# Performance work log

Hardware: AMD Instinct MI355X
Metric: run time of the kernel (lower is better)

## Reference

```python
import jax, jax.numpy as jnp
import numpy as np

NEG = -65504.0
D = 640


def _linear(x, W, b):
    return x @ W + b


def _qkv_attention(q, k, v, mask4):
    # q:[B,Lq,D] k,v:[B,Lk,D] mask4:[B,1,1,Lk] (True = masked)
    scores = jnp.einsum('bqd,bkd->bqk', q, k) / jnp.sqrt(jnp.asarray(q.shape[-1], q.dtype))
    scores = jnp.where(mask4[:, 0, :, :], NEG, scores)  # mask.squeeze(1) -> [B,1,Lk]
    p = jax.nn.softmax(scores, axis=-1)
    return jnp.einsum('bqk,bkd->bqd', p, v)


def _attflat(x, mask4, W1, b1, W2, b2, Wm, bm):
    # x:[B,N,D]; glimpses == 1
    att = _linear(jax.nn.relu(_linear(x, W1, b1)), W2, b2)  # [B,N,1]
    m = mask4[:, 0, 0, :, None]                              # [B,N,1]
    att = jnp.where(m, NEG, att)
    att = jax.nn.softmax(att, axis=1)
    pooled = jnp.sum(att * x, axis=1)                        # [B,D]
    return _linear(pooled, Wm, bm), att[..., 0]              # att.squeeze() -> [B,N]


def setup_inputs() -> dict:
    key = jax.random.key(0)
    ks = jax.random.split(key, 16)
    B, Ni, Nq = 64, 512, 128
    s = 0.02
    inp = {
        'i_batch': jax.random.normal(ks[0], (B, Ni, D), jnp.float32),
        'q_batch': jax.random.normal(ks[1], (B, Nq, D), jnp.float32),
        'i_mask': jax.random.bernoulli(ks[2], 0.3, (B, 1, 1, Ni)),
        'q_mask': jax.random.bernoulli(ks[3], 0.3, (B, 1, 1, Nq)),
        # l_flatten params (applied to image-side features)
        'lW1': jax.random.normal(ks[4], (D, 2 * D), jnp.float32) * s,
        'lb1': jnp.zeros((2 * D,), jnp.float32),
        'lW2': jax.random.normal(ks[5], (2 * D, 1), jnp.float32) * s,
        'lb2': jnp.zeros((1,), jnp.float32),
        'lWm': jax.random.normal(ks[6], (D, D), jnp.float32) * s,
        'lbm': jnp.zeros((D,), jnp.float32),
        # i_flatten params (applied to language-side features)
        'iW1': jax.random.normal(ks[7], (D, 2 * D), jnp.float32) * s,
        'ib1': jnp.zeros((2 * D,), jnp.float32),
        'iW2': jax.random.normal(ks[8], (2 * D, 1), jnp.float32) * s,
        'ib2': jnp.zeros((1,), jnp.float32),
        'iWm': jax.random.normal(ks[9], (D, D), jnp.float32) * s,
        'ibm': jnp.zeros((D,), jnp.float32),
    }
    return inp


def reference(i_batch, q_batch, i_mask, q_mask,
              lW1, lb1, lW2, lb2, lWm, lbm,
              iW1, ib1, iW2, ib2, iWm, ibm):
    # image attends over question tokens
    i_feat = _qkv_attention(i_batch, q_batch, q_batch, q_mask)   # [B,Ni,D]
    i_feat, i_weight = _attflat(i_feat, i_mask, lW1, lb1, lW2, lb2, lWm, lbm)
    # question attends over image regions
    l_feat = _qkv_attention(q_batch, i_batch, i_batch, i_mask)   # [B,Nq,D]
    l_feat, _ = _attflat(l_feat, q_mask, iW1, ib1, iW2, ib2, iWm, ibm)
    return (i_feat, l_feat, i_weight)
```

## Files before the change

### kernel.cpp

```cpp
#include <hip/hip_runtime.h>
#include <cstdint>

#define DEV __device__ __forceinline__

typedef __attribute__((ext_vector_type(8))) short bf16x8;
typedef __attribute__((ext_vector_type(4))) float f32x4;

static constexpr int B  = 64;
static constexpr int NI = 512;
static constexpr int NQ = 128;
static constexpr int D  = 640;
static constexpr int H  = 1280;
static constexpr float NEGV  = -65504.0f;
static constexpr float SCALE = 0.039528470752104745f;

DEV unsigned short f2bf(float f) {
  union { float f; uint32_t u; } c; c.f = f;
  uint32_t u = c.u;
  u += 0x7fffu + ((u >> 16) & 1u);
  return (unsigned short)(u >> 16);
}
DEV float bf2f(unsigned short h) {
  union { uint32_t u; float f; } c; c.u = ((uint32_t)h) << 16;
  return c.f;
}

DEV int xcd_swz(int bid, int nwg) {
  return (bid & 7) * (nwg >> 3) + (bid >> 3);
}

DEV void gll16(const void* g, void* l) {
  __builtin_amdgcn_global_load_lds(
      (const __attribute__((address_space(1))) void*)(uintptr_t)g,
      (__attribute__((address_space(3))) void*)(uint32_t)(uintptr_t)l,
      16, 0, 0);
}

template<int ROWS>
DEV void stageT(const unsigned short* src, int ld, unsigned short* lds, int tid) {
  const int w = tid >> 6, lane = tid & 63;
#pragma unroll
  for (int i = 0; i < ROWS / 32; ++i) {
    int c = w * (ROWS * 2) + i * 64 + lane;
    int r = c >> 3, ck = c & 7;
    int col8 = ((ck ^ (r & 7)) << 3);
    gll16(src + (long)r * ld + col8, (char*)lds + (size_t)c * 16);
  }
}

DEV bf16x8 frag(const unsigned short* ls, int row, int q) {
  return *(const bf16x8*)&ls[row * 64 + ((q ^ (row & 7)) << 3)];
}
DEV bf16x8 fragP(const unsigned short* P, int row, int q) {
  return *(const bf16x8*)&P[row * 128 + ((q ^ (row & 7)) << 3)];
}

template<int OUT_BF16>
__global__ __launch_bounds__(256, 2) void gemm_nt(
    const unsigned short* __restrict__ A, const unsigned short* __restrict__ Bt,
    void* __restrict__ C, int lda, int ldb, int ldc, int K,
    long sA, long sB, long sC, int gx, int gy)
{
  __shared__ __align__(16) unsigned short lsA[2][128 * 64];
  __shared__ __align__(16) unsigned short lsB[2][128 * 64];
  const int tid = threadIdx.x;
  const int w = tid >> 6, lane = tid & 63;
  const int wm = w >> 1, wn = w & 1;
  const int g = lane >> 4, r = lane & 15;
  const int wg = xcd_swz(blockIdx.x, gridDim.x);
  const int bz = wg / (gx * gy);
  const int r2 = wg - bz * gx * gy;
  const int by = r2 / gx;
  const int bx = r2 - by * gx;
  const long zb = bz;
  const unsigned short* Ab = A + zb * sA + (long)bx * 128 * lda;
  const unsigned short* Bb = Bt + zb * sB + (long)by * 128 * ldb;

  const int nt = K >> 6;
  stageT<128>(Ab, lda, lsA[0], tid);
  stageT<128>(Bb, ldb, lsB[0], tid);
  f32x4 acc[4][4] = {};
  for (int t = 0; t < nt; ++t) {
    __syncthreads();
    if (t + 1 < nt) {
      stageT<128>(Ab + (t + 1) * 64, lda, lsA[(t + 1) & 1], tid);
      stageT<128>(Bb + (t + 1) * 64, ldb, lsB[(t + 1) & 1], tid);
    }
    const unsigned short* la = lsA[t & 1];
    const unsigned short* lb = lsB[t & 1];
#pragma unroll
    for (int kk = 0; kk < 2; ++kk) {
      bf16x8 af[4], bfr[4];
#pragma unroll
      for (int mi = 0; mi < 4; ++mi) af[mi]  = frag(la, wm * 64 + mi * 16 + r, kk * 4 + g);
#pragma unroll
      for (int ni = 0; ni < 4; ++ni) bfr[ni] = frag(lb, wn * 64 + ni * 16 + r, kk * 4 + g);
#pragma unroll
      for (int mi = 0; mi < 4; ++mi)
#pragma unroll
        for (int ni = 0; ni < 4; ++ni)
          acc[mi][ni] = __builtin_amdgcn_mfma_f32_16x16x32_bf16(af[mi], bfr[ni], acc[mi][ni], 0, 0, 0);
    }
  }
  const int row0 = bx * 128 + wm * 64;
  const int col0 = by * 128 + wn * 64;
#pragma unroll
  for (int mi = 0; mi < 4; ++mi)
#pragma unroll
    for (int ni = 0; ni < 4; ++ni)
#pragma unroll
      for (int j = 0; j < 4; ++j) {
        int rr = row0 + mi * 16 + g * 4 + j;
        int cc = col0 + ni * 16 + r;
        float v = acc[mi][ni][j];
        if (OUT_BF16)
          ((unsigned short*)C)[zb * sC + (long)rr * ldc + cc] = f2bf(v);
        else
          ((float*)C)[zb * sC + (long)rr * ldc + cc] = v;
      }
}

__global__ __launch_bounds__(256, 2) void fattn1_k(
    const unsigned short* __restrict__ Qm,
    const unsigned short* __restrict__ Km,
    const unsigned short* __restrict__ Vt,
    const int* __restrict__ mask,
    unsigned short* __restrict__ O)
{
  __shared__ __align__(16) unsigned short sh[64 * 64 + 128 * 64];
  __shared__ __align__(16) unsigned short lsV[2][128 * 64];
  __shared__ float red0[64][2], red1[64][2];
  unsigned short* lsQ = sh;
  unsigned short* lsK = sh + 64 * 64;
  unsigned short* Pl  = sh;
  const int tid = threadIdx.x;
  const int w = tid >> 6, lane = tid & 63;
  const int wm = w >> 1, wn = w & 1;
  const int g = lane >> 4, r = lane & 15;
  const int wg = xcd_swz(blockIdx.x, gridDim.x);
  const int mt = wg & 7, b = wg >> 3;
  const unsigned short* Qb = Qm + ((long)b * NI + (long)mt * 64) * D;
  const unsigned short* Kb = Km + (long)b * NQ * D;
  const unsigned short* Vb = Vt + (long)b * D * NQ;

  int mki[4];
#pragma unroll
  for (int ni = 0; ni < 4; ++ni) mki[ni] = mask[b * NQ + wn * 64 + ni * 16 + r];

  f32x4 acc[2][4] = {};
  for (int k0 = 0; k0 < D; k0 += 64) {
    stageT<64>(Qb + k0, D, lsQ, tid);
    stageT<128>(Kb + k0, D, lsK, tid);
    __syncthreads();
#pragma unroll
    for (int kk = 0; kk < 2; ++kk) {
      bf16x8 af[2], bfr[4];
#pragma unroll
      for (int mi = 0; mi < 2; ++mi) af[mi]  = frag(lsQ, wm * 32 + mi * 16 + r, kk * 4 + g);
#pragma unroll
      for (int ni = 0; ni < 4; ++ni) bfr[ni] = frag(lsK, wn * 64 + ni * 16 + r, kk * 4 + g);
#pragma unroll
      for (int mi = 0; mi < 2; ++mi)
#pragma unroll
        for (int ni = 0; ni < 4; ++ni)
          acc[mi][ni] = __builtin_amdgcn_mfma_f32_16x16x32_bf16(af[mi], bfr[ni], acc[mi][ni], 0, 0, 0);
    }
    __syncthreads();
  }

  float x[2][4][4], pm[2][4];
#pragma unroll
  for (int mi = 0; mi < 2; ++mi)
#pragma unroll
    for (int j = 0; j < 4; ++j) pm[mi][j] = -3.4e38f;
#pragma unroll
  for (int mi = 0; mi < 2; ++mi)
#pragma unroll
    for (int ni = 0; ni < 4; ++ni)
#pragma unroll
      for (int j = 0; j < 4; ++j) {
        float v = mki[ni] ? NEGV : acc[mi][ni][j] * SCALE;
        x[mi][ni][j] = v;
        pm[mi][j] = fmaxf(pm[mi][j], v);
      }
#pragma unroll
  for (int s = 1; s < 16; s <<= 1)
#pragma unroll
    for (int mi = 0; mi < 2; ++mi)
#pragma unroll
      for (int j = 0; j < 4; ++j) pm[mi][j] = fmaxf(pm[mi][j], __shfl_xor(pm[mi][j], s));
  if (r == 0) {
#pragma unroll
    for (int mi = 0; mi < 2; ++mi)
#pragma unroll
      for (int j = 0; j < 4; ++j) red0[wm * 32 + mi * 16 + g * 4 + j][wn] = pm[mi][j];
  }
  __syncthreads();
  float mx[2][4], ps[2][4];
#pragma unroll
  for (int mi = 0; mi < 2; ++mi)
#pragma unroll
    for (int j = 0; j < 4; ++j) {
      int rl = wm * 32 + mi * 16 + g * 4 + j;
      mx[mi][j] = fmaxf(red0[rl][0], red0[rl][1]);
      ps[mi][j] = 0.f;
    }
#pragma unroll
  for (int mi = 0; mi < 2; ++mi)
#pragma unroll
    for (int ni = 0; ni < 4; ++ni)
#pragma unroll
      for (int j = 0; j < 4; ++j) {
        float e = __expf(x[mi][ni][j] - mx[mi][j]);
        x[mi][ni][j] = e;
        ps[mi][j] += e;
      }
#pragma unroll
  for (int s = 1; s < 16; s <<= 1)
#pragma unroll
    for (int mi = 0; mi < 2; ++mi)
#pragma unroll
      for (int j = 0; j < 4; ++j) ps[mi][j] += __shfl_xor(ps[mi][j], s);
  if (r == 0) {
#pragma unroll
    for (int mi = 0; mi < 2; ++mi)
#pragma unroll
      for (int j = 0; j < 4; ++j) red1[wm * 32 + mi * 16 + g * 4 + j][wn] = ps[mi][j];
  }
  __syncthreads();
#pragma unroll
  for (int mi = 0; mi < 2; ++mi)
#pragma unroll
    for (int j = 0; j < 4; ++j) {
      int rl = wm * 32 + mi * 16 + g * 4 + j;
      float inv = 1.f / (red1[rl][0] + red1[rl][1]);
#pragma unroll
      for (int ni = 0; ni < 4; ++ni) {
        int col = wn * 64 + ni * 16 + r;
        Pl[rl * 128 + (((col >> 3) ^ (rl & 7)) << 3) + (col & 7)] = f2bf(x[mi][ni][j] * inv);
      }
    }
  stageT<128>(Vb, 128, lsV[0], tid);
  stageT<128>(Vb + 64, 128, lsV[1], tid);
  __syncthreads();

  for (int nc = 0; nc < 5; ++nc) {
    if (nc > 0) __syncthreads();
    f32x4 po[2][4] = {};
#pragma unroll
    for (int kk2 = 0; kk2 < 2; ++kk2)
#pragma unroll
      for (int kk = 0; kk < 2; ++kk) {
        bf16x8 af[2], bfr[4];
#pragma unroll
        for (int mi = 0; mi < 2; ++mi) af[mi]  = fragP(Pl, wm * 32 + mi * 16 + r, kk2 * 8 + kk * 4 + g);
#pragma unroll
        for (int ni = 0; ni < 4; ++ni) bfr[ni] = frag(lsV[kk2], wn * 64 + ni * 16 + r, kk * 4 + g);
#pragma unroll
        for (int mi = 0; mi < 2; ++mi)
#pragma unroll
          for (int ni = 0; ni < 4; ++ni)
            po[mi][ni] = __builtin_amdgcn_mfma_f32_16x16x32_bf16(af[mi], bfr[ni], po[mi][ni], 0, 0, 0);
      }
    __syncthreads();
    if (nc < 4) {
      const unsigned short* Vn = Vb + (long)(nc + 1) * 128 * 128;
      stageT<128>(Vn, 128, lsV[0], tid);
      stageT<128>(Vn + 64, 128, lsV[1], tid);
    }
#pragma unroll
    for (int mi = 0; mi < 2; ++mi)
#pragma unroll
      for (int ni = 0; ni < 4; ++ni)
#pragma unroll
        for (int j = 0; j < 4; ++j) {
          int rr = mt * 64 + wm * 32 + mi * 16 + g * 4 + j;
          int cc = nc * 128 + wn * 64 + ni * 16 + r;
          O[((long)b * NI + rr) * D + cc] = f2bf(po[mi][ni][j]);
        }
  }
}

__global__ __launch_bounds__(256, 2) void hatt_k(
    const unsigned short* __restrict__ A, const unsigned short* __restrict__ Bt,
    const float* __restrict__ b1, const float* __restrict__ W2,
    float* __restrict__ outlogit)
{
  constexpr int NH = H / 128;
  __shared__ __align__(16) unsigned short lsA[2][128 * 64];
  __shared__ __align__(16) unsigned short lsB[2][128 * 64];
  __shared__ float b1c[128], w2c[128];
  const int tid = threadIdx.x;
  const int w = tid >> 6, lane = tid & 63;
  const int wm = w >> 1, wn = w & 1;
  const int g = lane >> 4, r = lane & 15;
  const int wg = xcd_swz(blockIdx.x, gridDim.x);
  const int n0 = (wg % NH) * 128;
  const int m0 = (wg / NH) * 128;
  if (tid < 128) { b1c[tid] = b1[n0 + tid]; w2c[tid] = W2[n0 + tid]; }
  const unsigned short* Ab = A + (long)m0 * D;
  const unsigned short* Bb = Bt + (long)n0 * D;

  constexpr int NT = D / 64;
  stageT<128>(Ab, D, lsA[0], tid);
  stageT<128>(Bb, D, lsB[0], tid);
  f32x4 acc[4][4] = {};
  for (int t = 0; t < NT; ++t) {
    __syncthreads();
    if (t + 1 < NT) {
      stageT<128>(Ab + (t + 1) * 64, D, lsA[(t + 1) & 1], tid);
      stageT<128>(Bb + (t + 1) * 64, D, lsB[(t + 1) & 1], tid);
    }
    const unsigned short* la = lsA[t & 1];
    const unsigned short* lb = lsB[t & 1];
#pragma unroll
    for (int kk = 0; kk < 2; ++kk) {
      bf16x8 af[4], bfr[4];
#pragma unroll
      for (int mi = 0; mi < 4; ++mi) af[mi]  = frag(la, wm * 64 + mi * 16 + r, kk * 4 + g);
#pragma unroll
      for (int ni = 0; ni < 4; ++ni) bfr[ni] = frag(lb, wn * 64 + ni * 16 + r, kk * 4 + g);
#pragma unroll
      for (int mi = 0; mi < 4; ++mi)
#pragma unroll
        for (int ni = 0; ni < 4; ++ni)
          acc[mi][ni] = __builtin_amdgcn_mfma_f32_16x16x32_bf16(af[mi], bfr[ni], acc[mi][ni], 0, 0, 0);
    }
  }
  float rs[4][4];
#pragma unroll
  for (int mi = 0; mi < 4; ++mi)
#pragma unroll
    for (int j = 0; j < 4; ++j) rs[mi][j] = 0.f;
#pragma unroll
  for (int mi = 0; mi < 4; ++mi)
#pragma unroll
    for (int ni = 0; ni < 4; ++ni)
#pragma unroll
      for (int j = 0; j < 4; ++j) {
        int cl = wn * 64 + ni * 16 + r;
        float h = acc[mi][ni][j] + b1c[cl];
        h = fmaxf(h, 0.f);
        rs[mi][j] += h * w2c[cl];
      }
#pragma unroll
  for (int mi = 0; mi < 4; ++mi)
#pragma unroll
    for (int j = 0; j < 4; ++j) {
      float v = rs[mi][j];
      v += __shfl_xor(v, 1); v += __shfl_xor(v, 2);
      v += __shfl_xor(v, 4); v += __shfl_xor(v, 8);
      if (r == 0) atomicAdd(&outlogit[m0 + wm * 64 + mi * 16 + g * 4 + j], v);
    }
}

template<int L>
__global__ void sm_scores(const float* __restrict__ S, const int* __restrict__ mask,
                          unsigned short* __restrict__ P, int M)
{
  constexpr int NV = L / 64;
  const int wid = threadIdx.x >> 6, lane = threadIdx.x & 63;
  const long row = (long)blockIdx.x * 4 + wid;
  const int b = (int)(row / M);
  const float* s = S + row * (long)L;
  const int* mk = mask + (long)b * L;
  float x[NV];
  float mx = -__builtin_inff();
#pragma unroll
  for (int i = 0; i < NV; ++i) {
    int idx = i * 64 + lane;
    float v = s[idx] * SCALE;
    x[i] = mk[idx] ? NEGV : v;
    mx = fmaxf(mx, x[i]);
  }
#pragma unroll
  for (int sft = 32; sft >= 1; sft >>= 1) mx = fmaxf(mx, __shfl_xor(mx, sft));
  float sum = 0.f;
#pragma unroll
  for (int i = 0; i < NV; ++i) { x[i] = __expf(x[i] - mx); sum += x[i]; }
#pragma unroll
  for (int sft = 32; sft >= 1; sft >>= 1) sum += __shfl_xor(sum, sft);
  const float inv = 1.f / sum;
  unsigned short* p = P + row * (long)L;
#pragma unroll
  for (int i = 0; i < NV; ++i) p[i * 64 + lane] = f2bf(x[i] * inv);
}

template<int L>
__global__ __launch_bounds__(640, 1) void tail_k(
    const float* __restrict__ logit, const int* __restrict__ mask,
    const float* __restrict__ b2p, const unsigned short* __restrict__ X,
    const float* __restrict__ Wm, const float* __restrict__ bm,
    float* __restrict__ outF, float* __restrict__ iw)
{
  __shared__ float att[L];
  __shared__ float pool[D];
  __shared__ float red[10];
  const int tid = threadIdx.x, b = blockIdx.x;
  const int lane = tid & 63, wv = tid >> 6;
  const float b2v = b2p[0];
  float v = -__builtin_inff();
  if (tid < L) v = mask[(long)b * L + tid] ? NEGV : (logit[(long)b * L + tid] + b2v);
  float m = v;
#pragma unroll
  for (int s = 32; s >= 1; s >>= 1) m = fmaxf(m, __shfl_xor(m, s));
  if (lane == 0) red[wv] = m;
  __syncthreads();
  float mx = red[0];
#pragma unroll
  for (int i = 1; i < 10; ++i) mx = fmaxf(mx, red[i]);
  __syncthreads();
  float e = (tid < L) ? __expf(v - mx) : 0.f;
  float ssum = e;
#pragma unroll
  for (int s = 32; s >= 1; s >>= 1) ssum += __shfl_xor(ssum, s);
  if (lane == 0) red[wv] = ssum;
  __syncthreads();
  float tot = 0.f;
#pragma unroll
  for (int i = 0; i < 10; ++i) tot += red[i];
  const float a = e / tot;
  if (tid < L) { att[tid] = a; if (iw) iw[(long)b * L + tid] = a; }
  __syncthreads();
  const unsigned short* Xb = X + (long)b * L * D + tid;
  float s = 0.f;
  for (int m2 = 0; m2 < L; ++m2) s += att[m2] * bf2f(Xb[(long)m2 * D]);
  pool[tid] = s;
  __syncthreads();
  float o = bm[tid];
  for (int k = 0; k < D; ++k) o += pool[k] * Wm[(long)k * D + tid];
  outF[(long)b * D + tid] = o;
}

template<int WRITE_N>
__global__ void cast_t_k(const float* __restrict__ in, unsigned short* __restrict__ outN,
                         unsigned short* __restrict__ outT, int R, int C)
{
  __shared__ float t[64][65];
  const int tid = threadIdx.x;
  const int cg = tid & 15, rw = tid >> 4;
  const long base = (long)blockIdx.z * R * C;
  const int c0 = blockIdx.x * 64, r0 = blockIdx.y * 64;
#pragma unroll
  for (int p = 0; p < 4; ++p) {
    int row = p * 16 + rw;
    float4 v = *(const float4*)&in[base + (long)(r0 + row) * C + c0 + cg * 4];
    *(float4*)&t[row][cg * 4] = v;
    if (WRITE_N) {
      ushort4 o;
      o.x = f2bf(v.x); o.y = f2bf(v.y); o.z = f2bf(v.z); o.w = f2bf(v.w);
      *(ushort4*)&outN[base + (long)(r0 + row) * C + c0 + cg * 4] = o;
    }
  }
  __syncthreads();
#pragma unroll
  for (int p = 0; p < 4; ++p) {
    int ocol = p * 16 + rw;
    ushort4 o;
    o.x = f2bf(t[cg * 4 + 0][ocol]);
    o.y = f2bf(t[cg * 4 + 1][ocol]);
    o.z = f2bf(t[cg * 4 + 2][ocol]);
    o.w = f2bf(t[cg * 4 + 3][ocol]);
    *(ushort4*)&outT[base + (long)(c0 + ocol) * R + r0 + cg * 4] = o;
  }
}

extern "C" void kernel_launch(void* const* d_in, const int* in_sizes, int n_in,
                              void* d_out, int out_size, void* d_ws, size_t ws_size,
                              hipStream_t stream)
{
  (void)in_sizes; (void)n_in; (void)out_size; (void)ws_size;
  const float* i_batch = (const float*)d_in[0];
  const float* q_batch = (const float*)d_in[1];
  const int*   i_mask  = (const int*)d_in[2];
  const int*   q_mask  = (const int*)d_in[3];
  const float* lW1 = (const float*)d_in[4];
  const float* lb1 = (const float*)d_in[5];
  const float* lW2 = (const float*)d_in[6];
  const float* lb2 = (const float*)d_in[7];
  const float* lWm = (const float*)d_in[8];
  const float* lbm = (const float*)d_in[9];
  const float* iW1 = (const float*)d_in[10];
  const float* ib1 = (const float*)d_in[11];
  const float* iW2 = (const float*)d_in[12];
  const float* ib2 = (const float*)d_in[13];
  const float* iWm = (const float*)d_in[14];
  const float* ibm = (const float*)d_in[15];
  float* out_if = (float*)d_out;
  float* out_lf = out_if + B * D;
  float* out_iw = out_lf + B * D;

  char* wp = (char*)d_ws;
  size_t off = 0;
  auto alloc = [&](size_t bytes) { void* p = wp + off; off += (bytes + 255) & ~(size_t)255; return p; };
  unsigned short* i_bf   = (unsigned short*)alloc((size_t)B * NI * D * 2);
  unsigned short* i_bfT  = (unsigned short*)alloc((size_t)B * NI * D * 2);
  unsigned short* q_bf   = (unsigned short*)alloc((size_t)B * NQ * D * 2);
  unsigned short* q_bfT  = (unsigned short*)alloc((size_t)B * NQ * D * 2);
  unsigned short* x1_bf  = (unsigned short*)alloc((size_t)B * NI * D * 2);
  unsigned short* x2_bf  = (unsigned short*)alloc((size_t)B * NQ * D * 2);
  float*          scores = (float*)alloc((size_t)B * NQ * NI * 4);
  unsigned short* p_bf   = (unsigned short*)alloc((size_t)B * NQ * NI * 2);
  unsigned short* lW1t   = (unsigned short*)alloc((size_t)H * D * 2);
  unsigned short* iW1t   = (unsigned short*)alloc((size_t)H * D * 2);
  float* logit1 = (float*)alloc((size_t)B * NI * 4);
  float* logit2 = (float*)alloc((size_t)B * NQ * 4);

  hipMemsetAsync(logit1, 0, (size_t)(B * NI + B * NQ) * 4, stream);

  cast_t_k<1><<<dim3(D / 64, NI / 64, B), 256, 0, stream>>>(i_batch, i_bf, i_bfT, NI, D);
  cast_t_k<1><<<dim3(D / 64, NQ / 64, B), 256, 0, stream>>>(q_batch, q_bf, q_bfT, NQ, D);
  cast_t_k<0><<<dim3(H / 64, D / 64, 1), 256, 0, stream>>>(lW1, nullptr, lW1t, D, H);
  cast_t_k<0><<<dim3(H / 64, D / 64, 1), 256, 0, stream>>>(iW1, nullptr, iW1t, D, H);

  fattn1_k<<<dim3(8 * B), 256, 0, stream>>>(i_bf, q_bf, q_bfT, q_mask, x1_bf);
  hatt_k<<<dim3((H / 128) * (B * NI / 128)), 256, 0, stream>>>(x1_bf, lW1t, lb1, lW2, logit1);
  tail_k<NI><<<dim3(B), 640, 0, stream>>>(logit1, i_mask, lb2, x1_bf, lWm, lbm, out_if, out_iw);

  gemm_nt<0><<<dim3((NQ / 128) * (NI / 128) * B), 256, 0, stream>>>(
      q_bf, i_bf, scores, D, D, NI, D, (long)NQ * D, (long)NI * D, (long)NQ * NI,
      NQ / 128, NI / 128);
  sm_scores<NI><<<dim3(B * NQ / 4), 256, 0, stream>>>(scores, i_mask, p_bf, NQ);
  gemm_nt<1><<<dim3((NQ / 128) * (D / 128) * B), 256, 0, stream>>>(
      p_bf, i_bfT, x2_bf, NI, NI, D, NI, (long)NQ * NI, (long)D * NI, (long)NQ * D,
      NQ / 128, D / 128);
  hatt_k<<<dim3((H / 128) * (B * NQ / 128)), 256, 0, stream>>>(x2_bf, iW1t, ib1, iW2, logit2);
  tail_k<NQ><<<dim3(B), 640, 0, stream>>>(logit2, q_mask, ib2, x2_bf, iWm, ibm, out_lf, nullptr);
}
```

Measured before the change: 427.3 us.

## Shrink GEMM K-tile to 32 for higher occupancy and split tail into parallel kernels

The batched GEMM and the fused hidden-attention GEMM now stage 32-wide K tiles with a 4-way swizzle instead of 64-wide ones. This halves LDS use so launch bounds can allow 4 blocks per CU. The pooling/projection tail used one 640-thread block per batch. It is now two kernels spread over a (B, D/128) grid, with each kernel splitting its reduction across 4 thread groups, which raises parallelism in the serial tail. The cost is twice as many K-loop barriers, a softmax recomputed in each of the 5 column blocks, and an extra launch plus a round trip through global memory for the pooled vector.

```diff
diff --git a/kernel.cpp b/kernel.cpp
--- a/kernel.cpp
+++ b/kernel.cpp
@@ -47,7 +47,6 @@
     gll16(src + (long)r * ld + col8, (char*)lds + (size_t)c * 16);
   }
 }
-
 DEV bf16x8 frag(const unsigned short* ls, int row, int q) {
   return *(const bf16x8*)&ls[row * 64 + ((q ^ (row & 7)) << 3)];
 }
@@ -55,14 +54,27 @@
   return *(const bf16x8*)&P[row * 128 + ((q ^ (row & 7)) << 3)];
 }
 
+DEV void stage32(const unsigned short* src, int ld, unsigned short* lds, int tid) {
+#pragma unroll
+  for (int i = 0; i < 2; ++i) {
+    int c = i * 256 + tid;
+    int r = c >> 2, ck = c & 3;
+    int col8 = ((ck ^ (r & 3)) << 3);
+    gll16(src + (long)r * ld + col8, (char*)lds + (size_t)c * 16);
+  }
+}
+DEV bf16x8 frag32(const unsigned short* ls, int row, int q) {
+  return *(const bf16x8*)&ls[row * 32 + ((q ^ (row & 3)) << 3)];
+}
+
 template<int OUT_BF16>
-__global__ __launch_bounds__(256, 2) void gemm_nt(
+__global__ __launch_bounds__(256, 4) void gemm_nt(
     const unsigned short* __restrict__ A, const unsigned short* __restrict__ Bt,
     void* __restrict__ C, int lda, int ldb, int ldc, int K,
     long sA, long sB, long sC, int gx, int gy)
 {
-  __shared__ __align__(16) unsigned short lsA[2][128 * 64];
-  __shared__ __align__(16) unsigned short lsB[2][128 * 64];
+  __shared__ __align__(16) unsigned short lsA[2][128 * 32];
+  __shared__ __align__(16) unsigned short lsB[2][128 * 32];
   const int tid = threadIdx.x;
   const int w = tid >> 6, lane = tid & 63;
   const int wm = w >> 1, wn = w & 1;
@@ -76,31 +88,28 @@
   const unsigned short* Ab = A + zb * sA + (long)bx * 128 * lda;
   const unsigned short* Bb = Bt + zb * sB + (long)by * 128 * ldb;
 
-  const int nt = K >> 6;
-  stageT<128>(Ab, lda, lsA[0], tid);
-  stageT<128>(Bb, ldb, lsB[0], tid);
+  const int nt = K >> 5;
+  stage32(Ab, lda, lsA[0], tid);
+  stage32(Bb, ldb, lsB[0], tid);
   f32x4 acc[4][4] = {};
   for (int t = 0; t < nt; ++t) {
     __syncthreads();
     if (t + 1 < nt) {
-      stageT<128>(Ab + (t + 1) * 64, lda, lsA[(t + 1) & 1], tid);
-      stageT<128>(Bb + (t + 1) * 64, ldb, lsB[(t + 1) & 1], tid);
+      stage32(Ab + (t + 1) * 32, lda, lsA[(t + 1) & 1], tid);
+      stage32(Bb + (t + 1) * 32, ldb, lsB[(t + 1) & 1], tid);
     }
     const unsigned short* la = lsA[t & 1];
     const unsigned short* lb = lsB[t & 1];
-#pragma unroll
-    for (int kk = 0; kk < 2; ++kk) {
-      bf16x8 af[4], bfr[4];
-#pragma unroll
-      for (int mi = 0; mi < 4; ++mi) af[mi]  = frag(la, wm * 64 + mi * 16 + r, kk * 4 + g);
-#pragma unroll
-      for (int ni = 0; ni < 4; ++ni) bfr[ni] = frag(lb, wn * 64 + ni * 16 + r, kk * 4 + g);
-#pragma unroll
-      for (int mi = 0; mi < 4; ++mi)
-#pragma unroll
-        for (int ni = 0; ni < 4; ++ni)
-          acc[mi][ni] = __builtin_amdgcn_mfma_f32_16x16x32_bf16(af[mi], bfr[ni], acc[mi][ni], 0, 0, 0);
-    }
+    bf16x8 af[4], bfr[4];
+#pragma unroll
+    for (int mi = 0; mi < 4; ++mi) af[mi]  = frag32(la, wm * 64 + mi * 16 + r, g);
+#pragma unroll
+    for (int ni = 0; ni < 4; ++ni) bfr[ni] = frag32(lb, wn * 64 + ni * 16 + r, g);
+#pragma unroll
+    for (int mi = 0; mi < 4; ++mi)
+#pragma unroll
+      for (int ni = 0; ni < 4; ++ni)
+        acc[mi][ni] = __builtin_amdgcn_mfma_f32_16x16x32_bf16(af[mi], bfr[ni], acc[mi][ni], 0, 0, 0);
   }
   const int row0 = bx * 128 + wm * 64;
   const int col0 = by * 128 + wn * 64;
@@ -118,6 +127,76 @@
         else
           ((float*)C)[zb * sC + (long)rr * ldc + cc] = v;
       }
+}
+
+__global__ __launch_bounds__(256, 4) void hatt_k(
+    const unsigned short* __restrict__ A, const unsigned short* __restrict__ Bt,
+    const float* __restrict__ b1, const float* __restrict__ W2,
+    float* __restrict__ outlogit)
+{
+  constexpr int NH = H / 128;
+  __shared__ __align__(16) unsigned short lsA[2][128 * 32];
+  __shared__ __align__(16) unsigned short lsB[2][128 * 32];
+  __shared__ float b1c[128], w2c[128];
+  const int tid = threadIdx.x;
+  const int w = tid >> 6, lane = tid & 63;
+  const int wm = w >> 1, wn = w & 1;
+  const int g = lane >> 4, r = lane & 15;
+  const int wg = xcd_swz(blockIdx.x, gridDim.x);
+  const int n0 = (wg % NH) * 128;
+  const int m0 = (wg / NH) * 128;
+  if (tid < 128) { b1c[tid] = b1[n0 + tid]; w2c[tid] = W2[n0 + tid]; }
+  const unsigned short* Ab = A + (long)m0 * D;
+  const unsigned short* Bb = Bt + (long)n0 * D;
+
+  constexpr int NT = D / 32;
+  stage32(Ab, D, lsA[0], tid);
+  stage32(Bb, D, lsB[0], tid);
+  f32x4 acc[4][4] = {};
+  for (int t = 0; t < NT; ++t) {
+    __syncthreads();
+    if (t + 1 < NT) {
+      stage32(Ab + (t + 1) * 32, D, lsA[(t + 1) & 1], tid);
+      stage32(Bb + (t + 1) * 32, D, lsB[(t + 1) & 1], tid);
+    }
+    const unsigned short* la = lsA[t & 1];
+    const unsigned short* lb = lsB[t & 1];
+    bf16x8 af[4], bfr[4];
+#pragma unroll
+    for (int mi = 0; mi < 4; ++mi) af[mi]  = frag32(la, wm * 64 + mi * 16 + r, g);
+#pragma unroll
+    for (int ni = 0; ni < 4; ++ni) bfr[ni] = frag32(lb, wn * 64 + ni * 16 + r, g);
+#pragma unroll
+    for (int mi = 0; mi < 4; ++mi)
+#pragma unroll
+      for (int ni = 0; ni < 4; ++ni)
+        acc[mi][ni] = __builtin_amdgcn_mfma_f32_16x16x32_bf16(af[mi], bfr[ni], acc[mi][ni], 0, 0, 0);
+  }
+  float rs[4][4];
+#pragma unroll
+  for (int mi = 0; mi < 4; ++mi)
+#pragma unroll
+    for (int j = 0; j < 4; ++j) rs[mi][j] = 0.f;
+#pragma unroll
+  for (int mi = 0; mi < 4; ++mi)
+#pragma unroll
+    for (int ni = 0; ni < 4; ++ni)
+#pragma unroll
+      for (int j = 0; j < 4; ++j) {
+        int cl = wn * 64 + ni * 16 + r;
+        float h = acc[mi][ni][j] + b1c[cl];
+        h = fmaxf(h, 0.f);
+        rs[mi][j] += h * w2c[cl];
+      }
+#pragma unroll
+  for (int mi = 0; mi < 4; ++mi)
+#pragma unroll
+    for (int j = 0; j < 4; ++j) {
+      float v = rs[mi][j];
+      v += __shfl_xor(v, 1); v += __shfl_xor(v, 2);
+      v += __shfl_xor(v, 4); v += __shfl_xor(v, 8);
+      if (r == 0) atomicAdd(&outlogit[m0 + wm * 64 + mi * 16 + g * 4 + j], v);
+    }
 }
 
 __global__ __launch_bounds__(256, 2) void fattn1_k(
@@ -281,79 +360,6 @@
   }
 }
 
-__global__ __launch_bounds__(256, 2) void hatt_k(
-    const unsigned short* __restrict__ A, const unsigned short* __restrict__ Bt,
-    const float* __restrict__ b1, const float* __restrict__ W2,
-    float* __restrict__ outlogit)
-{
-  constexpr int NH = H / 128;
-  __shared__ __align__(16) unsigned short lsA[2][128 * 64];
-  __shared__ __align__(16) unsigned short lsB[2][128 * 64];
-  __shared__ float b1c[128], w2c[128];
-  const int tid = threadIdx.x;
-  const int w = tid >> 6, lane = tid & 63;
-  const int wm = w >> 1, wn = w & 1;
-  const int g = lane >> 4, r = lane & 15;
-  const int wg = xcd_swz(blockIdx.x, gridDim.x);
-  const int n0 = (wg % NH) * 128;
-  const int m0 = (wg / NH) * 128;
-  if (tid < 128) { b1c[tid] = b1[n0 + tid]; w2c[tid] = W2[n0 + tid]; }
-  const unsigned short* Ab = A + (long)m0 * D;
-  const unsigned short* Bb = Bt + (long)n0 * D;
-
-  constexpr int NT = D / 64;
-  stageT<128>(Ab, D, lsA[0], tid);
-  stageT<128>(Bb, D, lsB[0], tid);
-  f32x4 acc[4][4] = {};
-  for (int t = 0; t < NT; ++t) {
-    __syncthreads();
-    if (t + 1 < NT) {
-      stageT<128>(Ab + (t + 1) * 64, D, lsA[(t + 1) & 1], tid);
-      stageT<128>(Bb + (t + 1) * 64, D, lsB[(t + 1) & 1], tid);
-    }
-    const unsigned short* la = lsA[t & 1];
-    const unsigned short* lb = lsB[t & 1];
-#pragma unroll
-    for (int kk = 0; kk < 2; ++kk) {
-      bf16x8 af[4], bfr[4];
-#pragma unroll
-      for (int mi = 0; mi < 4; ++mi) af[mi]  = frag(la, wm * 64 + mi * 16 + r, kk * 4 + g);
-#pragma unroll
-      for (int ni = 0; ni < 4; ++ni) bfr[ni] = frag(lb, wn * 64 + ni * 16 + r, kk * 4 + g);
-#pragma unroll
-      for (int mi = 0; mi < 4; ++mi)
-#pragma unroll
-        for (int ni = 0; ni < 4; ++ni)
-          acc[mi][ni] = __builtin_amdgcn_mfma_f32_16x16x32_bf16(af[mi], bfr[ni], acc[mi][ni], 0, 0, 0);
-    }
-  }
-  float rs[4][4];
-#pragma unroll
-  for (int mi = 0; mi < 4; ++mi)
-#pragma unroll
-    for (int j = 0; j < 4; ++j) rs[mi][j] = 0.f;
-#pragma unroll
-  for (int mi = 0; mi < 4; ++mi)
-#pragma unroll
-    for (int ni = 0; ni < 4; ++ni)
-#pragma unroll
-      for (int j = 0; j < 4; ++j) {
-        int cl = wn * 64 + ni * 16 + r;
-        float h = acc[mi][ni][j] + b1c[cl];
-        h = fmaxf(h, 0.f);
-        rs[mi][j] += h * w2c[cl];
-      }
-#pragma unroll
-  for (int mi = 0; mi < 4; ++mi)
-#pragma unroll
-    for (int j = 0; j < 4; ++j) {
-      float v = rs[mi][j];
-      v += __shfl_xor(v, 1); v += __shfl_xor(v, 2);
-      v += __shfl_xor(v, 4); v += __shfl_xor(v, 8);
-      if (r == 0) atomicAdd(&outlogit[m0 + wm * 64 + mi * 16 + g * 4 + j], v);
-    }
-}
-
 template<int L>
 __global__ void sm_scores(const float* __restrict__ S, const int* __restrict__ mask,
                           unsigned short* __restrict__ P, int M)
@@ -387,15 +393,14 @@
 }
 
 template<int L>
-__global__ __launch_bounds__(640, 1) void tail_k(
+__global__ __launch_bounds__(512, 2) void tail1_k(
     const float* __restrict__ logit, const int* __restrict__ mask,
     const float* __restrict__ b2p, const unsigned short* __restrict__ X,
-    const float* __restrict__ Wm, const float* __restrict__ bm,
-    float* __restrict__ outF, float* __restrict__ iw)
+    float* __restrict__ pooled, float* __restrict__ iw)
 {
   __shared__ float att[L];
-  __shared__ float pool[D];
-  __shared__ float red[10];
+  __shared__ float red[8];
+  __shared__ float part[4][128];
   const int tid = threadIdx.x, b = blockIdx.x;
   const int lane = tid & 63, wv = tid >> 6;
   const float b2v = b2p[0];
@@ -408,7 +413,7 @@
   __syncthreads();
   float mx = red[0];
 #pragma unroll
-  for (int i = 1; i < 10; ++i) mx = fmaxf(mx, red[i]);
+  for (int i = 1; i < 8; ++i) mx = fmaxf(mx, red[i]);
   __syncthreads();
   float e = (tid < L) ? __expf(v - mx) : 0.f;
   float ssum = e;
@@ -418,18 +423,47 @@
   __syncthreads();
   float tot = 0.f;
 #pragma unroll
-  for (int i = 0; i < 10; ++i) tot += red[i];
+  for (int i = 0; i < 8; ++i) tot += red[i];
   const float a = e / tot;
-  if (tid < L) { att[tid] = a; if (iw) iw[(long)b * L + tid] = a; }
-  __syncthreads();
-  const unsigned short* Xb = X + (long)b * L * D + tid;
+  if (tid < L) {
+    att[tid] = a;
+    if (iw && blockIdx.y == 0) iw[(long)b * L + tid] = a;
+  }
+  __syncthreads();
+  const int d = blockIdx.y * 128 + (tid & 127);
+  const int grp = tid >> 7;
+  const unsigned short* Xb = X + (long)b * L * D + d;
   float s = 0.f;
-  for (int m2 = 0; m2 < L; ++m2) s += att[m2] * bf2f(Xb[(long)m2 * D]);
-  pool[tid] = s;
-  __syncthreads();
-  float o = bm[tid];
-  for (int k = 0; k < D; ++k) o += pool[k] * Wm[(long)k * D + tid];
-  outF[(long)b * D + tid] = o;
+  const int m0 = grp * (L / 4);
+#pragma unroll 4
+  for (int m2 = m0; m2 < m0 + L / 4; ++m2) s += att[m2] * bf2f(Xb[(long)m2 * D]);
+  part[grp][tid & 127] = s;
+  __syncthreads();
+  if (tid < 128)
+    pooled[(long)b * D + blockIdx.y * 128 + tid] =
+        part[0][tid] + part[1][tid] + part[2][tid] + part[3][tid];
+}
+
+__global__ __launch_bounds__(512, 2) void tail2_k(
+    const float* __restrict__ pooled, const float* __restrict__ W,
+    const float* __restrict__ bias, float* __restrict__ out)
+{
+  __shared__ float p[D];
+  __shared__ float part[4][128];
+  const int tid = threadIdx.x, b = blockIdx.x;
+  const int n = blockIdx.y * 128 + (tid & 127);
+  const int kg = tid >> 7;
+  for (int i = tid; i < D; i += 512) p[i] = pooled[(long)b * D + i];
+  __syncthreads();
+  float acc = 0.f;
+  const int k0 = kg * (D / 4);
+#pragma unroll 4
+  for (int k = k0; k < k0 + D / 4; ++k) acc += p[k] * W[(long)k * D + n];
+  part[kg][tid & 127] = acc;
+  __syncthreads();
+  if (tid < 128)
+    out[(long)b * D + blockIdx.y * 128 + tid] =
+        bias[blockIdx.y * 128 + tid] + part[0][tid] + part[1][tid] + part[2][tid] + part[3][tid];
 }
 
 template<int WRITE_N>
@@ -503,8 +537,10 @@
   unsigned short* p_bf   = (unsigned short*)alloc((size_t)B * NQ * NI * 2);
   unsigned short* lW1t   = (unsigned short*)alloc((size_t)H * D * 2);
   unsigned short* iW1t   = (unsigned short*)alloc((size_t)H * D * 2);
-  float* logit1 = (float*)alloc((size_t)B * NI * 4);
-  float* logit2 = (float*)alloc((size_t)B * NQ * 4);
+  float* logit1  = (float*)alloc((size_t)B * NI * 4);
+  float* logit2  = (float*)alloc((size_t)B * NQ * 4);
+  float* pooled1 = (float*)alloc((size_t)B * D * 4);
+  float* pooled2 = (float*)alloc((size_t)B * D * 4);
 
   hipMemsetAsync(logit1, 0, (size_t)(B * NI + B * NQ) * 4, stream);
 
@@ -515,7 +551,8 @@
 
   fattn1_k<<<dim3(8 * B), 256, 0, stream>>>(i_bf, q_bf, q_bfT, q_mask, x1_bf);
   hatt_k<<<dim3((H / 128) * (B * NI / 128)), 256, 0, stream>>>(x1_bf, lW1t, lb1, lW2, logit1);
-  tail_k<NI><<<dim3(B), 640, 0, stream>>>(logit1, i_mask, lb2, x1_bf, lWm, lbm, out_if, out_iw);
+  tail1_k<NI><<<dim3(B, D / 128), 512, 0, stream>>>(logit1, i_mask, lb2, x1_bf, pooled1, out_iw);
+  tail2_k<<<dim3(B, D / 128), 512, 0, stream>>>(pooled1, lWm, lbm, out_if);
 
   gemm_nt<0><<<dim3((NQ / 128) * (NI / 128) * B), 256, 0, stream>>>(
       q_bf, i_bf, scores, D, D, NI, D, (long)NQ * D, (long)NI * D, (long)NQ * NI,
@@ -525,5 +562,6 @@
       p_bf, i_bfT, x2_bf, NI, NI, D, NI, (long)NQ * NI, (long)D * NI, (long)NQ * D,
       NQ / 128, D / 128);
   hatt_k<<<dim3((H / 128) * (B * NQ / 128)), 256, 0, stream>>>(x2_bf, iW1t, ib1, iW2, logit2);
-  tail_k<NQ><<<dim3(B), 640, 0, stream>>>(logit2, q_mask, ib2, x2_bf, iWm, ibm, out_lf, nullptr);
-}
+  tail1_k<NQ><<<dim3(B, D / 128), 512, 0, stream>>>(logit2, q_mask, ib2, x2_bf, pooled2, nullptr);
+  tail2_k<<<dim3(B, D / 128), 512, 0, stream>>>(pooled2, iWm, ibm, out_lf);
+}
```

After: 419.0 us. About the same (-1.9%).
